# Performance work log

Measured on AMD Instinct MI355X. Metric: run time of the kernel, lower is better.

The kernel has to match this reference:

```python
import jax, jax.numpy as jnp
import numpy as np

WS = 8      # window_size
NH = 6      # num_heads
SHIFT = 4   # shift_size


def setup_inputs() -> dict:
    key = jax.random.key(0)
    k0, k1, k2, k3, k4 = jax.random.split(key, 5)
    B, C, H, W = 4, 192, 224, 224
    x = jax.random.normal(k0, (B, C, H, W), jnp.float32)
    # 1x1 convs == per-pixel linear layers: store weights as (out, in)
    w_qkv = jax.random.normal(k1, (3 * C, C), jnp.float32) * 0.05
    b_qkv = jax.random.normal(k2, (3 * C,), jnp.float32) * 0.05
    w_proj = jax.random.normal(k3, (C, C), jnp.float32) * 0.05
    b_proj = jax.random.normal(k4, (C,), jnp.float32) * 0.05
    return {"x": x, "w_qkv": w_qkv, "b_qkv": b_qkv, "w_proj": w_proj, "b_proj": b_proj}


def reference(x, w_qkv, b_qkv, w_proj, b_proj):
    B, C, H, W = x.shape
    hd = C // NH
    scale = hd ** -0.5

    if SHIFT > 0:
        x = jnp.roll(x, shift=(-SHIFT, -SHIFT), axis=(2, 3))

    pad_r = (WS - W % WS) % WS
    pad_b = (WS - H % WS) % WS
    if pad_r > 0 or pad_b > 0:
        x = jnp.pad(x, ((0, 0), (0, 0), (0, pad_b), (0, pad_r)))
    Hp, Wp = x.shape[2], x.shape[3]
    Hn, Wn = Hp // WS, Wp // WS

    # qkv 1x1 conv: (B,C,Hp,Wp) -> (B,3C,Hp,Wp)
    qkv = jnp.einsum('bchw,oc->bohw', x, w_qkv) + b_qkv[None, :, None, None]

    # (B,3,NH,hd,Hn,WS,Wn,WS) -> (3,B,Hn,Wn,NH,WS,WS,hd)
    qkv = qkv.reshape(B, 3, NH, hd, Hn, WS, Wn, WS)
    qkv = jnp.transpose(qkv, (1, 0, 4, 6, 2, 5, 7, 3))
    q = qkv[0].reshape(-1, NH, WS * WS, hd)  # (B*Hn*Wn, NH, 64, hd)
    k = qkv[1].reshape(-1, NH, WS * WS, hd)
    v = qkv[2].reshape(-1, NH, WS * WS, hd)

    attn = jax.nn.softmax(jnp.einsum('wnqd,wnkd->wnqk', q, k) * scale, axis=-1)
    out = jnp.einsum('wnqk,wnkd->wnqd', attn, v)

    # (B,Hn,Wn,NH,WS,WS,hd) -> (B,NH,hd,Hn,WS,Wn,WS) -> (B,C,Hp,Wp)
    out = out.reshape(B, Hn, Wn, NH, WS, WS, hd)
    out = jnp.transpose(out, (0, 3, 6, 1, 4, 2, 5)).reshape(B, C, Hp, Wp)

    out = jnp.einsum('bchw,oc->bohw', out, w_proj) + b_proj[None, :, None, None]

    if pad_r > 0 or pad_b > 0:
        out = out[:, :, :H, :W]
    if SHIFT > 0:
        out = jnp.roll(out, shift=(SHIFT, SHIFT), axis=(2, 3))
    return out
```

## Files before the change

kernel.cpp:

```cpp
#include <hip/hip_runtime.h>
#include <stdint.h>

#define HHW   224
#define CCH   192
#define SHIFT 4
#define NWIN  3136
#define NTOK  200704
#define QN    38535168ull

typedef __attribute__((ext_vector_type(8))) short bf16x8;
typedef __attribute__((ext_vector_type(4))) float f32x4;

__device__ __forceinline__ ushort f2bf(float f) {
    union { float f; uint32_t i; } v; v.f = f;
    uint32_t u = v.i;
    return (ushort)((u + 0x7FFFu + ((u >> 16) & 1u)) >> 16);
}

__global__ __launch_bounds__(256) void prep_w(const float* __restrict__ w,
                                              ushort* __restrict__ wo, int nrow)
{
    int idx = blockIdx.x * 256 + threadIdx.x;
    if (idx >= nrow * 24) return;
    int rg = idx / 24, p = idx % 24;
    int s = p ^ (rg & 7);
    const float* src = w + (size_t)rg * 192 + s * 8;
    float4 a = *(const float4*)src;
    float4 b = *(const float4*)(src + 4);
    uint4 o;
    o.x = (uint32_t)f2bf(a.x) | ((uint32_t)f2bf(a.y) << 16);
    o.y = (uint32_t)f2bf(a.z) | ((uint32_t)f2bf(a.w) << 16);
    o.z = (uint32_t)f2bf(b.x) | ((uint32_t)f2bf(b.y) << 16);
    o.w = (uint32_t)f2bf(b.z) | ((uint32_t)f2bf(b.w) << 16);
    *(uint4*)(wo + (size_t)rg * 192 + p * 8) = o;
}

__global__ __launch_bounds__(256) void prep_x(const float* __restrict__ x,
                                              ushort* __restrict__ xo)
{
    __shared__ ushort xt[64][200];
    const int win = blockIdx.x;
    const int b = win / 784, hn = (win / 28) % 28, wn = win % 28;
    const float* xb = x + (size_t)b * CCH * HHW * HHW;

    for (int u = threadIdx.x; u < CCH * 16; u += 256) {
        int c = u >> 4, r = u & 15;
        int t0 = r * 4;
        int hh = (hn * 8 + (t0 >> 3) + SHIFT) % HHW;
        int ww = (wn * 8 + (t0 & 7) + SHIFT) % HHW;
        float4 v = *(const float4*)(xb + ((size_t)c * HHW + hh) * HHW + ww);
        xt[t0 + 0][c] = f2bf(v.x); xt[t0 + 1][c] = f2bf(v.y);
        xt[t0 + 2][c] = f2bf(v.z); xt[t0 + 3][c] = f2bf(v.w);
    }
    __syncthreads();
    ushort* xw = xo + (size_t)win * 12288;
    for (int u = threadIdx.x; u < 64 * 24; u += 256) {
        int t = u / 24, c8 = u % 24;
        *(uint4*)(xw + t * 192 + c8 * 8) = *(const uint4*)&xt[t][c8 * 8];
    }
}

template<int OCH>
__global__ __launch_bounds__(256, 3) void gemm_win(
    const ushort* __restrict__ xin, const ushort* __restrict__ wbf,
    const float* __restrict__ bias,
    ushort* __restrict__ qo, ushort* __restrict__ ko, ushort* __restrict__ vto,
    float* __restrict__ dout)
{
    __shared__ ushort wc[96 * 192];

    const int tid = threadIdx.x;
    const int wave = tid >> 6, lane = tid & 63;
    const int quad = lane >> 4, l16 = lane & 15;
    const int p0 = blockIdx.x * 128 + wave * 32;

    #pragma unroll
    for (int it = 0; it < 9; it++) {
        int off = (it * 4 + wave) * 512;
        __builtin_amdgcn_global_load_lds(
            (const __attribute__((address_space(1))) void*)(wbf + off + lane * 8),
            (__attribute__((address_space(3))) void*)(&wc[off]), 16, 0, 0);
    }

    bf16x8 bfr[2][6];
    #pragma unroll
    for (int nt = 0; nt < 2; nt++)
        #pragma unroll
        for (int k = 0; k < 6; k++)
            bfr[nt][k] = *(const bf16x8*)(xin + (size_t)(p0 + nt * 16 + l16) * CCH + k * 32 + quad * 8);

    __syncthreads();

    #pragma unroll
    for (int ch = 0; ch < OCH / 96; ch++) {
        f32x4 acc[6][2];
        #pragma unroll
        for (int m = 0; m < 6; m++)
            #pragma unroll
            for (int nt = 0; nt < 2; nt++) acc[m][nt] = (f32x4){0.f, 0.f, 0.f, 0.f};

        const ushort* wl = wc + (size_t)l16 * 192;
        #pragma unroll
        for (int k = 0; k < 6; k++) {
            const ushort* wk = wl + ((k * 4 + quad) ^ (l16 & 7)) * 8;
            #pragma unroll
            for (int m = 0; m < 6; m++) {
                bf16x8 afrag = *(const bf16x8*)(wk + m * 3072);
                acc[m][0] = __builtin_amdgcn_mfma_f32_16x16x32_bf16(afrag, bfr[0][k], acc[m][0], 0, 0, 0);
                acc[m][1] = __builtin_amdgcn_mfma_f32_16x16x32_bf16(afrag, bfr[1][k], acc[m][1], 0, 0, 0);
            }
        }

        if (ch + 1 < OCH / 96) {
            __syncthreads();
            const ushort* wsrc = wbf + (size_t)(ch + 1) * (96 * 192);
            #pragma unroll
            for (int it = 0; it < 9; it++) {
                int off = (it * 4 + wave) * 512;
                __builtin_amdgcn_global_load_lds(
                    (const __attribute__((address_space(1))) void*)(wsrc + off + lane * 8),
                    (__attribute__((address_space(3))) void*)(&wc[off]), 16, 0, 0);
            }
        }

        const int obase = ch * 96;
        #pragma unroll
        for (int m = 0; m < 6; m++) {
            const int o0 = obase + m * 16 + quad * 4;
            float4 bb = *(const float4*)(bias + o0);
            #pragma unroll
            for (int nt = 0; nt < 2; nt++) {
                int token = p0 + nt * 16 + l16;
                int win = token >> 6, t = token & 63;
                float f0 = acc[m][nt][0] + bb.x, f1 = acc[m][nt][1] + bb.y;
                float f2 = acc[m][nt][2] + bb.z, f3 = acc[m][nt][3] + bb.w;
                if (OCH == 576) {
                    const int s = o0 / 192;
                    const int rem = o0 % 192;
                    const int h = rem >> 5, d0 = rem & 31;
                    size_t wh = (size_t)win * 6 + h;
                    if (s == 2) {
                        vto[(wh * 32 + d0 + 0) * 64 + t] = f2bf(f0);
                        vto[(wh * 32 + d0 + 1) * 64 + t] = f2bf(f1);
                        vto[(wh * 32 + d0 + 2) * 64 + t] = f2bf(f2);
                        vto[(wh * 32 + d0 + 3) * 64 + t] = f2bf(f3);
                    } else {
                        uint2 pk;
                        pk.x = (uint32_t)f2bf(f0) | ((uint32_t)f2bf(f1) << 16);
                        pk.y = (uint32_t)f2bf(f2) | ((uint32_t)f2bf(f3) << 16);
                        ushort* dst = (s == 0 ? qo : ko) + (wh * 64 + t) * 32 + d0;
                        *(uint2*)dst = pk;
                    }
                } else {
                    int b = win / 784, hn = (win / 28) % 28, wn = win % 28;
                    int hh = (hn * 8 + (t >> 3) + SHIFT) % HHW;
                    int ww = (wn * 8 + (t & 7) + SHIFT) % HHW;
                    float* dst = dout + ((size_t)(b * CCH + o0) * HHW + hh) * HHW + ww;
                    dst[0] = f0; dst[(size_t)HHW * HHW] = f1;
                    dst[2 * (size_t)HHW * HHW] = f2; dst[3 * (size_t)HHW * HHW] = f3;
                }
            }
        }
        if (ch + 1 < OCH / 96) __syncthreads();
    }
}

__global__ __launch_bounds__(384, 3) void attn_win(
    ushort* qx2,
    const ushort* __restrict__ k, const ushort* __restrict__ vt)
{
    __shared__ ushort pt[6][64][72];

    const int tid = threadIdx.x;
    const int h = tid >> 6, lane = tid & 63;
    const int quad = lane >> 4, l16 = lane & 15;
    const int win = blockIdx.x;

    const ushort* qp = qx2 + (size_t)(win * 6 + h) * 2048;
    const ushort* kp = k   + (size_t)(win * 6 + h) * 2048;
    const ushort* vp = vt  + (size_t)(win * 6 + h) * 2048;

    bf16x8 kf[4], vf[2][2];
    #pragma unroll
    for (int nt = 0; nt < 4; nt++) kf[nt] = *(const bf16x8*)&kp[(nt * 16 + l16) * 32 + quad * 8];
    #pragma unroll
    for (int ks = 0; ks < 2; ks++)
        #pragma unroll
        for (int nt = 0; nt < 2; nt++)
            vf[ks][nt] = *(const bf16x8*)&vp[(nt * 16 + l16) * 64 + ks * 32 + quad * 8];

    f32x4 s[4][4];
    #pragma unroll
    for (int mt = 0; mt < 4; mt++) {
        bf16x8 qf = *(const bf16x8*)&qp[(mt * 16 + l16) * 32 + quad * 8];
        #pragma unroll
        for (int nt = 0; nt < 4; nt++) {
            s[mt][nt] = (f32x4){0.f, 0.f, 0.f, 0.f};
            s[mt][nt] = __builtin_amdgcn_mfma_f32_16x16x32_bf16(qf, kf[nt], s[mt][nt], 0, 0, 0);
        }
    }

    const float SC = 0.25506953149031837f;
    #pragma unroll
    for (int mt = 0; mt < 4; mt++) {
        #pragma unroll
        for (int rg = 0; rg < 4; rg++) {
            float v0 = s[mt][0][rg], v1 = s[mt][1][rg], v2 = s[mt][2][rg], v3 = s[mt][3][rg];
            float mx = fmaxf(fmaxf(v0, v1), fmaxf(v2, v3));
            #pragma unroll
            for (int msk = 1; msk < 16; msk <<= 1) mx = fmaxf(mx, __shfl_xor(mx, msk, 64));
            float e0 = exp2f((v0 - mx) * SC), e1 = exp2f((v1 - mx) * SC);
            float e2 = exp2f((v2 - mx) * SC), e3 = exp2f((v3 - mx) * SC);
            float sm = (e0 + e1) + (e2 + e3);
            #pragma unroll
            for (int msk = 1; msk < 16; msk <<= 1) sm += __shfl_xor(sm, msk, 64);
            float r = __builtin_amdgcn_rcpf(sm);
            int qt = mt * 16 + quad * 4 + rg;
            pt[h][qt][ 0 + l16] = f2bf(e0 * r);
            pt[h][qt][16 + l16] = f2bf(e1 * r);
            pt[h][qt][32 + l16] = f2bf(e2 * r);
            pt[h][qt][48 + l16] = f2bf(e3 * r);
        }
    }
    __syncthreads();

    f32x4 o[4][2];
    #pragma unroll
    for (int mt = 0; mt < 4; mt++)
        #pragma unroll
        for (int nt = 0; nt < 2; nt++) o[mt][nt] = (f32x4){0.f, 0.f, 0.f, 0.f};
    #pragma unroll
    for (int ks = 0; ks < 2; ks++)
        #pragma unroll
        for (int mt = 0; mt < 4; mt++) {
            bf16x8 pf = *(const bf16x8*)&pt[h][mt * 16 + l16][ks * 32 + quad * 8];
            #pragma unroll
            for (int nt = 0; nt < 2; nt++)
                o[mt][nt] = __builtin_amdgcn_mfma_f32_16x16x32_bf16(pf, vf[ks][nt], o[mt][nt], 0, 0, 0);
        }

    ushort* x2 = qx2 + (size_t)win * 12288;
    #pragma unroll
    for (int mt = 0; mt < 4; mt++)
        #pragma unroll
        for (int nt = 0; nt < 2; nt++)
            #pragma unroll
            for (int rg = 0; rg < 4; rg++) {
                int qt = mt * 16 + quad * 4 + rg;
                x2[qt * CCH + h * 32 + nt * 16 + l16] = f2bf(o[mt][nt][rg]);
            }
}

extern "C" void kernel_launch(void* const* d_in, const int* in_sizes, int n_in,
                              void* d_out, int out_size, void* d_ws, size_t ws_size,
                              hipStream_t stream) {
    const float* x      = (const float*)d_in[0];
    const float* w_qkv  = (const float*)d_in[1];
    const float* b_qkv  = (const float*)d_in[2];
    const float* w_proj = (const float*)d_in[3];
    const float* b_proj = (const float*)d_in[4];
    float* out = (float*)d_out;
    ushort* ws = (ushort*)d_ws;

    ushort* X1 = (ushort*)d_out;
    ushort* WQ = (ushort*)d_out + QN;
    ushort* Q  = ws;
    ushort* K  = ws + QN;
    ushort* VT = ws + 2 * QN;
    ushort* WP = VT;

    prep_w       <<<54, 256, 0, stream>>>(w_qkv, WQ, 576);
    prep_x       <<<NWIN, 256, 0, stream>>>(x, X1);
    gemm_win<576><<<NTOK / 128, 256, 0, stream>>>(X1, WQ, b_qkv, Q, K, VT, nullptr);
    attn_win     <<<NWIN, 384, 0, stream>>>(Q, K, VT);
    prep_w       <<<18, 256, 0, stream>>>(w_proj, WP, 192);
    gemm_win<192><<<NTOK / 128, 256, 0, stream>>>(Q, WP, b_proj, nullptr, nullptr, nullptr, out);
}
```

Measured before the change: 629.2 us.

## Restructure input prep into channel-octet blocks with swizzled LDS and new window layout

```diff
diff --git a/kernel.cpp b/kernel.cpp
--- a/kernel.cpp
+++ b/kernel.cpp
@@ -15,6 +15,9 @@
     union { float f; uint32_t i; } v; v.f = f;
     uint32_t u = v.i;
     return (ushort)((u + 0x7FFFu + ((u >> 16) & 1u)) >> 16);
+}
+__device__ __forceinline__ uint32_t pk2(float a, float b) {
+    return (uint32_t)f2bf(a) | ((uint32_t)f2bf(b) << 16);
 }
 
 __global__ __launch_bounds__(256) void prep_w(const float* __restrict__ w,
@@ -28,35 +31,50 @@
     float4 a = *(const float4*)src;
     float4 b = *(const float4*)(src + 4);
     uint4 o;
-    o.x = (uint32_t)f2bf(a.x) | ((uint32_t)f2bf(a.y) << 16);
-    o.y = (uint32_t)f2bf(a.z) | ((uint32_t)f2bf(a.w) << 16);
-    o.z = (uint32_t)f2bf(b.x) | ((uint32_t)f2bf(b.y) << 16);
-    o.w = (uint32_t)f2bf(b.z) | ((uint32_t)f2bf(b.w) << 16);
+    o.x = pk2(a.x, a.y); o.y = pk2(a.z, a.w);
+    o.z = pk2(b.x, b.y); o.w = pk2(b.z, b.w);
     *(uint4*)(wo + (size_t)rg * 192 + p * 8) = o;
 }
 
 __global__ __launch_bounds__(256) void prep_x(const float* __restrict__ x,
                                               ushort* __restrict__ xo)
 {
-    __shared__ ushort xt[64][200];
-    const int win = blockIdx.x;
-    const int b = win / 784, hn = (win / 28) % 28, wn = win % 28;
-    const float* xb = x + (size_t)b * CCH * HHW * HHW;
-
-    for (int u = threadIdx.x; u < CCH * 16; u += 256) {
-        int c = u >> 4, r = u & 15;
-        int t0 = r * 4;
-        int hh = (hn * 8 + (t0 >> 3) + SHIFT) % HHW;
-        int ww = (wn * 8 + (t0 & 7) + SHIFT) % HHW;
-        float4 v = *(const float4*)(xb + ((size_t)c * HHW + hh) * HHW + ww);
-        xt[t0 + 0][c] = f2bf(v.x); xt[t0 + 1][c] = f2bf(v.y);
-        xt[t0 + 2][c] = f2bf(v.z); xt[t0 + 3][c] = f2bf(v.w);
+    __shared__ ushort lt[1792 * 8];
+    const int blk = blockIdx.x;
+    const int oct = blk % 24;
+    const int bh  = blk / 24;
+    const int hn  = bh % 28;
+    const float* xb = x + ((size_t)(bh / 28) * CCH + oct * 8) * (HHW * HHW);
+
+    for (int u = threadIdx.x; u < 448; u += 256) {
+        int r = u / 56, q = u % 56;
+        int hh = (hn * 8 + r + SHIFT) % HHW;
+        int ww = (q * 4 + SHIFT) % HHW;
+        const float* src = xb + (size_t)hh * HHW + ww;
+        float4 v[8];
+        #pragma unroll
+        for (int c = 0; c < 8; c++)
+            v[c] = *(const float4*)(src + (size_t)c * (HHW * HHW));
+        #pragma unroll
+        for (int i = 0; i < 4; i++) {
+            int p = u * 4 + i;
+            int sw = p ^ ((p >> 3) & 7);
+            uint4 o;
+            o.x = pk2(((const float*)&v[0])[i], ((const float*)&v[1])[i]);
+            o.y = pk2(((const float*)&v[2])[i], ((const float*)&v[3])[i]);
+            o.z = pk2(((const float*)&v[4])[i], ((const float*)&v[5])[i]);
+            o.w = pk2(((const float*)&v[6])[i], ((const float*)&v[7])[i]);
+            *(uint4*)&lt[sw * 8] = o;
+        }
     }
     __syncthreads();
-    ushort* xw = xo + (size_t)win * 12288;
-    for (int u = threadIdx.x; u < 64 * 24; u += 256) {
-        int t = u / 24, c8 = u % 24;
-        *(uint4*)(xw + t * 192 + c8 * 8) = *(const uint4*)&xt[t][c8 * 8];
+
+    for (int u = threadIdx.x; u < 1792; u += 256) {
+        int wn = u >> 6, t = u & 63;
+        int p = (t >> 3) * 224 + wn * 8 + (t & 7);
+        int sw = p ^ ((p >> 3) & 7);
+        *(uint4*)(xo + (size_t)(bh * 28 + wn) * 12288 + oct * 512 + t * 8) =
+            *(const uint4*)&lt[sw * 8];
     }
 }
 
@@ -84,10 +102,17 @@
 
     bf16x8 bfr[2][6];
     #pragma unroll
-    for (int nt = 0; nt < 2; nt++)
-        #pragma unroll
-        for (int k = 0; k < 6; k++)
-            bfr[nt][k] = *(const bf16x8*)(xin + (size_t)(p0 + nt * 16 + l16) * CCH + k * 32 + quad * 8);
+    for (int nt = 0; nt < 2; nt++) {
+        int token = p0 + nt * 16 + l16;
+        #pragma unroll
+        for (int k = 0; k < 6; k++) {
+            if (OCH == 576)
+                bfr[nt][k] = *(const bf16x8*)(xin + (size_t)(token >> 6) * 12288
+                                              + (k * 4 + quad) * 512 + (token & 63) * 8);
+            else
+                bfr[nt][k] = *(const bf16x8*)(xin + (size_t)token * CCH + k * 32 + quad * 8);
+        }
+    }
 
     __syncthreads();
 
@@ -146,8 +171,8 @@
                         vto[(wh * 32 + d0 + 3) * 64 + t] = f2bf(f3);
                     } else {
                         uint2 pk;
-                        pk.x = (uint32_t)f2bf(f0) | ((uint32_t)f2bf(f1) << 16);
-                        pk.y = (uint32_t)f2bf(f2) | ((uint32_t)f2bf(f3) << 16);
+                        pk.x = pk2(f0, f1);
+                        pk.y = pk2(f2, f3);
                         ushort* dst = (s == 0 ? qo : ko) + (wh * 64 + t) * 32 + d0;
                         *(uint2*)dst = pk;
                     }
@@ -270,7 +295,7 @@
     ushort* WP = VT;
 
     prep_w       <<<54, 256, 0, stream>>>(w_qkv, WQ, 576);
-    prep_x       <<<NWIN, 256, 0, stream>>>(x, X1);
+    prep_x       <<<4 * 28 * 24, 256, 0, stream>>>(x, X1);
     gemm_win<576><<<NTOK / 128, 256, 0, stream>>>(X1, WQ, b_qkv, Q, K, VT, nullptr);
     attn_win     <<<NWIN, 384, 0, stream>>>(Q, K, VT);
     prep_w       <<<18, 256, 0, stream>>>(w_proj, WP, 192);
```

After: 564.8 us. 1.11x faster.
